# Performance work log

Measured on AMD Instinct MI355X. Metric: run time of the kernel, lower is better.

The kernel has to match this reference:

```python
import jax, jax.numpy as jnp
import numpy as np

N = 100000      # nodes
E = 3_200_000   # edges
F_IN = 256      # input feature dim
R = 16          # rank_bound (GCN output dim)
D = 128         # embedding_dim (trans output)
B = 16384       # batch of node indices
EPS = 1e-5


def setup_inputs() -> dict:
    key = jax.random.key(0)
    ks = jax.random.split(key, 9)
    x = jax.random.normal(ks[0], (N, F_IN), jnp.float32)
    edge_index = jax.random.randint(ks[1], (2, E), 0, N, dtype=jnp.int64)
    trans = jax.random.normal(ks[2], (R, D), jnp.float32) * 0.1
    batch = jax.random.randint(ks[3], (B,), 0, N, dtype=jnp.int64)
    W = jax.random.normal(ks[4], (R, F_IN), jnp.float32) / np.sqrt(F_IN).astype(np.float32)
    b = jnp.zeros((R,), jnp.float32)
    ln_w = jnp.ones((R,), jnp.float32)
    ln_b = jnp.zeros((R,), jnp.float32)
    prelu_a = jnp.full((1,), 0.25, jnp.float32)  # PReLU single shared slope
    return dict(x=x, edge_index=edge_index, trans=trans, batch=batch,
                W=W, b=b, ln_w=ln_w, ln_b=ln_b, prelu_a=prelu_a)


def gcn_conv(x, edge_index, W, b):
    # PyG GCNConv: lin first, then symmetric-normalized aggregation with self-loops.
    h = x @ W.T  # [N, R]
    loop = jnp.arange(N, dtype=edge_index.dtype)
    src = jnp.concatenate([edge_index[0], loop])  # messages flow src -> dst
    dst = jnp.concatenate([edge_index[1], loop])
    deg = jax.ops.segment_sum(jnp.ones_like(dst, h.dtype), dst, num_segments=N)
    dinv = jnp.where(deg > 0, jax.lax.rsqrt(deg), 0.0)
    norm = dinv[src] * dinv[dst]                   # [E+N]
    msg = h[src] * norm[:, None]                   # gather [E+N, R]
    out = jax.ops.segment_sum(msg, dst, num_segments=N)  # scatter-add
    return out + b


def reference(x, edge_index, trans, batch, W, b, ln_w, ln_b, prelu_a):
    h = gcn_conv(x, edge_index, W, b)              # [N, R]
    # PyG LayerNorm (graph mode): normalize over all nodes and channels.
    h = h - h.mean()
    var = (h * h).mean()
    h = h * jax.lax.rsqrt(var + EPS) * ln_w + ln_b
    # PReLU
    h = jnp.where(h >= 0, h, prelu_a * h)
    emb = h @ trans                                # [N, D]
    return emb[batch]                              # index_select(0, batch)
```

## Files before the change

### kernel.cpp

```cpp
#include <hip/hip_runtime.h>

#define EPS 1e-5f
#define BSHIFT 8
#define BSIZE  256
#define NBMAX  512
#define PCHUNK 8192
#define LCAP   12288

typedef short bf16x8 __attribute__((ext_vector_type(8)));
typedef float f32x4  __attribute__((ext_vector_type(4)));

__device__ __forceinline__ unsigned short f2bf(float f) {
    unsigned u = __float_as_uint(f);
    u += 0x7FFFu + ((u >> 16) & 1u);
    return (unsigned short)(u >> 16);
}
__device__ __forceinline__ float bf2f(unsigned short s) {
    return __uint_as_float(((unsigned)s) << 16);
}
__device__ __forceinline__ void acc8(float* acc, uint4 v) {
    acc[0] += bf2f((unsigned short)(v.x & 0xFFFFu)); acc[1] += bf2f((unsigned short)(v.x >> 16));
    acc[2] += bf2f((unsigned short)(v.y & 0xFFFFu)); acc[3] += bf2f((unsigned short)(v.y >> 16));
    acc[4] += bf2f((unsigned short)(v.z & 0xFFFFu)); acc[5] += bf2f((unsigned short)(v.z >> 16));
    acc[6] += bf2f((unsigned short)(v.w & 0xFFFFu)); acc[7] += bf2f((unsigned short)(v.w >> 16));
}
__device__ __forceinline__ void cvt_hilo(const float* f, bf16x8& hi, bf16x8& lo) {
#pragma unroll
    for (int j = 0; j < 8; j++) {
        unsigned short h = f2bf(f[j]);
        hi[j] = (short)h;
        lo[j] = (short)f2bf(f[j] - bf2f(h));
    }
}
__device__ __forceinline__ void gload_lds16(const float* g, float* l) {
    __builtin_amdgcn_global_load_lds((const __attribute__((address_space(1))) void*)g,
                                     (__attribute__((address_space(3))) void*)l, 16, 0, 0);
}

__global__ __launch_bounds__(512) void k_zero(unsigned* ghist, int NB) {
    int t = threadIdx.x;
    if (t < NB) ghist[t] = 0u;
}

__global__ __launch_bounds__(512) void k_bhist(const int* __restrict__ ei,
                                               unsigned* __restrict__ ghist,
                                               unsigned* __restrict__ blkhist,
                                               int E, int NB) {
    __shared__ unsigned sh[NBMAX];
    int t = threadIdx.x;
    for (int i = t; i < NB; i += 512) sh[i] = 0u;
    __syncthreads();
    const int4* dst4 = (const int4*)(ei + E);
    int E4 = E >> 2;
    int base4 = blockIdx.x * (PCHUNK / 4);
#pragma unroll
    for (int i = 0; i < PCHUNK / 4 / 512; i++) {
        int idx = base4 + i * 512 + t;
        if (idx < E4) {
            int4 d = dst4[idx];
            atomicAdd(&sh[d.x >> BSHIFT], 1u);
            atomicAdd(&sh[d.y >> BSHIFT], 1u);
            atomicAdd(&sh[d.z >> BSHIFT], 1u);
            atomicAdd(&sh[d.w >> BSHIFT], 1u);
        }
    }
    __syncthreads();
    unsigned* bh = blkhist + (size_t)blockIdx.x * NBMAX;
    for (int i = t; i < NB; i += 512) {
        unsigned c = sh[i];
        bh[i] = c;
        if (c) atomicAdd(&ghist[i], c);
    }
}

__global__ __launch_bounds__(512) void k_bscan(const unsigned* __restrict__ ghist,
                                               unsigned* __restrict__ base,
                                               unsigned* __restrict__ cursor,
                                               unsigned* __restrict__ nstart,
                                               int NB, int N, int E) {
    __shared__ unsigned sh[512];
    int t = threadIdx.x;
    unsigned v = (t < NB) ? ghist[t] : 0u;
    sh[t] = v;
    __syncthreads();
    for (int off = 1; off < 512; off <<= 1) {
        unsigned a = (t >= off) ? sh[t - off] : 0u;
        __syncthreads();
        sh[t] += a;
        __syncthreads();
    }
    if (t < NB) { unsigned ex = sh[t] - v; base[t] = ex; cursor[t] = ex; }
    if (t == 0) { base[NB] = (unsigned)E; nstart[N] = (unsigned)E; }
}

__global__ __launch_bounds__(512) void k_bpart(const int* __restrict__ ei,
                                               const unsigned* __restrict__ blkhist,
                                               unsigned* __restrict__ cursor,
                                               unsigned* __restrict__ sorted, int E, int NB) {
    __shared__ unsigned cnt[NBMAX];
    __shared__ unsigned lbase[NBMAX];
    __shared__ unsigned loff[NBMAX + 1];
    __shared__ unsigned sh[512];
    __shared__ unsigned stage[PCHUNK];
    __shared__ unsigned short bkt[PCHUNK];
    int t = threadIdx.x;
    const unsigned* bh = blkhist + (size_t)blockIdx.x * NBMAX;
    for (int i = t; i < NB; i += 512) cnt[i] = bh[i];
    __syncthreads();
    const int4* src4 = (const int4*)ei;
    const int4* dst4 = (const int4*)(ei + E);
    int E4 = E >> 2;
    int base4 = blockIdx.x * (PCHUNK / 4);
    unsigned v = (t < NB) ? cnt[t] : 0u;
    sh[t] = v;
    if (t < NB) lbase[t] = v ? atomicAdd(&cursor[t], v) : 0u;
    __syncthreads();
    for (int off = 1; off < 512; off <<= 1) {
        unsigned a = (t >= off) ? sh[t - off] : 0u;
        __syncthreads();
        sh[t] += a;
        __syncthreads();
    }
    if (t < NB) { loff[t] = sh[t] - v; cnt[t] = 0u; }
    if (t == NB - 1) loff[NB] = sh[t];
    __syncthreads();
    for (int b = t; b < NB; b += 512) {
        unsigned s = loff[b], e2 = loff[b + 1];
        for (unsigned j = s; j < e2; j++) bkt[j] = (unsigned short)b;
    }
#pragma unroll
    for (int i = 0; i < PCHUNK / 4 / 512; i++) {
        int idx = base4 + i * 512 + t;
        if (idx < E4) {
            int4 s = src4[idx];
            int4 d = dst4[idx];
            int b; unsigned r;
            b = d.x >> BSHIFT; r = atomicAdd(&cnt[b], 1u);
            stage[loff[b] + r] = (unsigned)s.x | ((unsigned)(d.x & (BSIZE - 1)) << 17);
            b = d.y >> BSHIFT; r = atomicAdd(&cnt[b], 1u);
            stage[loff[b] + r] = (unsigned)s.y | ((unsigned)(d.y & (BSIZE - 1)) << 17);
            b = d.z >> BSHIFT; r = atomicAdd(&cnt[b], 1u);
            stage[loff[b] + r] = (unsigned)s.z | ((unsigned)(d.z & (BSIZE - 1)) << 17);
            b = d.w >> BSHIFT; r = atomicAdd(&cnt[b], 1u);
            stage[loff[b] + r] = (unsigned)s.w | ((unsigned)(d.w & (BSIZE - 1)) << 17);
        }
    }
    __syncthreads();
    unsigned total = loff[NB];
    for (unsigned i = t; i < total; i += 512) {
        unsigned b = bkt[i];
        sorted[lbase[b] + (i - loff[b])] = stage[i];
    }
}

__global__ __launch_bounds__(256) void k_bdeg2(const unsigned* __restrict__ base,
                                               const unsigned* __restrict__ sorted,
                                               unsigned* __restrict__ nstart,
                                               float* __restrict__ dinv, int N) {
    __shared__ unsigned deg[BSIZE];
    int b = blockIdx.x, t = threadIdx.x;
    deg[t] = 0u;
    __syncthreads();
    unsigned s0 = base[b], s1 = base[b + 1];
    for (unsigned j = s0 + t; j < s1; j += 256)
        atomicAdd(&deg[sorted[j] >> 17], 1u);
    __syncthreads();
    unsigned d0 = deg[t];
    int lane = t & 63, wid = t >> 6;
    unsigned inc = d0;
    for (int off = 1; off < 64; off <<= 1) {
        unsigned u = __shfl_up(inc, off, 64);
        if (lane >= off) inc += u;
    }
    __shared__ unsigned wsum[4];
    if (lane == 63) wsum[wid] = inc;
    __syncthreads();
    unsigned wbase = 0;
    for (int w = 0; w < wid; w++) wbase += wsum[w];
    unsigned excl = wbase + inc - d0;
    int node = (b << BSHIFT) + t;
    if (node < N) {
        nstart[node] = s0 + excl;
        dinv[node] = rsqrtf((float)(d0 + 1u));
    }
}

__global__ __launch_bounds__(256) void k_gemm(const float* __restrict__ x,
                                              const float* __restrict__ W,
                                              const float* __restrict__ dinv,
                                              unsigned short* __restrict__ hs,
                                              int N, int NCH) {
    __shared__ float xs[64][260];
    int t = threadIdx.x;
    int w = t >> 6, lane = t & 63;
    int lr = lane & 15;
    int lk = lane >> 4;
    bf16x8 bh[8], bl[8];
#pragma unroll
    for (int kt = 0; kt < 8; kt++) {
        float wf[8];
        const float* wp = W + lr * 256 + kt * 32 + lk * 8;
        *(float4*)&wf[0] = *(const float4*)wp;
        *(float4*)&wf[4] = *(const float4*)(wp + 4);
        cvt_hilo(wf, bh[kt], bl[kt]);
    }
    for (int ch = blockIdx.x; ch < NCH; ch += gridDim.x) {
        int cb = ch << 6;
#pragma unroll
        for (int j = 0; j < 16; j++) {
            int row = w * 16 + j;
            int node = cb + row;
            if (node < N)
                gload_lds16(x + (size_t)node * 256 + lane * 4, &xs[row][0]);
        }
        __syncthreads();
        f32x4 acc = {0.f, 0.f, 0.f, 0.f};
#pragma unroll
        for (int kt = 0; kt < 8; kt++) {
            float af[8];
            const float* ap = &xs[w * 16 + lr][kt * 32 + lk * 8];
            *(float4*)&af[0] = *(const float4*)ap;
            *(float4*)&af[4] = *(const float4*)(ap + 4);
            bf16x8 ah, al;
            cvt_hilo(af, ah, al);
            acc = __builtin_amdgcn_mfma_f32_16x16x32_bf16(ah, bh[kt], acc, 0, 0, 0);
            acc = __builtin_amdgcn_mfma_f32_16x16x32_bf16(al, bh[kt], acc, 0, 0, 0);
            acc = __builtin_amdgcn_mfma_f32_16x16x32_bf16(ah, bl[kt], acc, 0, 0, 0);
        }
#pragma unroll
        for (int i = 0; i < 4; i++) {
            int node = cb + w * 16 + lk * 4 + i;
            if (node < N) {
                float dv = dinv[node];
                hs[(size_t)node * 16 + lr] = f2bf(acc[i] * dv);
            }
        }
        __syncthreads();
    }
}

__global__ __launch_bounds__(256) void k_aggf(const unsigned* __restrict__ base,
                                              const unsigned* __restrict__ nstart,
                                              const unsigned* __restrict__ sorted,
                                              const unsigned short* __restrict__ hs,
                                              const float* __restrict__ dinv,
                                              const float* __restrict__ bias,
                                              float* __restrict__ agg,
                                              float2* __restrict__ part,
                                              unsigned* __restrict__ scratch, int N) {
    __shared__ unsigned buf[LCAP];
    __shared__ unsigned cur0[BSIZE + 1];
    __shared__ unsigned curv[BSIZE];
    __shared__ float ss[4], qq[4];
    int b = blockIdx.x, t = threadIdx.x;
    unsigned s0 = base[b], s1 = base[b + 1];
    unsigned len = s1 - s0;
    int node = (b << BSHIFT) + t;
    unsigned ns = (node < N) ? nstart[node] : s1;
    cur0[t] = ns - s0;
    curv[t] = ns - s0;
    if (t == 0) cur0[BSIZE] = len;
    __syncthreads();
    bool fit = (len <= (unsigned)LCAP);
    if (fit) {
        for (unsigned j = t; j < len; j += 256) {
            unsigned u = sorted[s0 + j];
            unsigned pos = atomicAdd(&curv[u >> 17], 1u);
            buf[pos] = u & 0x1FFFFu;
        }
    } else {
        for (unsigned j = t; j < len; j += 256) {
            unsigned u = sorted[s0 + j];
            unsigned pos = atomicAdd(&curv[u >> 17], 1u);
            scratch[s0 + pos] = u & 0x1FFFFu;
        }
    }
    __syncthreads();
    int g = t >> 4, r = t & 15;
    int sub = r >> 1;
    int half = r & 1;
    float sacc = 0.f, qacc = 0.f;
#pragma unroll 1
    for (int p = 0; p < 16; p++) {
        int dloc = p * 16 + g;
        int d = (b << BSHIFT) + dloc;
        float acc[8];
#pragma unroll
        for (int c = 0; c < 8; c++) acc[c] = 0.f;
        if (d < N) {
            unsigned l0 = cur0[dloc], l1 = cur0[dloc + 1];
            for (unsigned j = l0; j < l1; j += 16) {
                unsigned row0 = j + sub, row1 = j + 8 + sub;
                bool p0 = row0 < l1, p1 = row1 < l1;
                unsigned i0 = 0, i1 = 0;
                if (fit) {
                    if (p0) i0 = buf[row0];
                    if (p1) i1 = buf[row1];
                } else {
                    if (p0) i0 = scratch[s0 + row0];
                    if (p1) i1 = scratch[s0 + row1];
                }
                uint4 v0, v1;
                if (p0) v0 = ((const uint4*)(hs + (size_t)i0 * 16))[half];
                if (p1) v1 = ((const uint4*)(hs + (size_t)i1 * 16))[half];
                if (p0) acc8(acc, v0);
                if (p1) acc8(acc, v1);
            }
        }
#pragma unroll
        for (int off = 2; off <= 8; off <<= 1) {
#pragma unroll
            for (int c = 0; c < 8; c++) acc[c] += __shfl_down(acc[c], off, 64);
        }
        if (d < N && r < 2) {
            float dd = dinv[d];
            uint4 hv = ((const uint4*)(hs + (size_t)d * 16))[half];
            float self[8];
            self[0] = bf2f((unsigned short)(hv.x & 0xFFFFu)); self[1] = bf2f((unsigned short)(hv.x >> 16));
            self[2] = bf2f((unsigned short)(hv.y & 0xFFFFu)); self[3] = bf2f((unsigned short)(hv.y >> 16));
            self[4] = bf2f((unsigned short)(hv.z & 0xFFFFu)); self[5] = bf2f((unsigned short)(hv.z >> 16));
            self[6] = bf2f((unsigned short)(hv.w & 0xFFFFu)); self[7] = bf2f((unsigned short)(hv.w >> 16));
            float o[8];
#pragma unroll
            for (int c = 0; c < 8; c++) o[c] = (acc[c] + self[c]) * dd;
            float* an = agg + (size_t)d * 16 + half * 8;
            *(float4*)(an)     = make_float4(o[0], o[1], o[2], o[3]);
            *(float4*)(an + 4) = make_float4(o[4], o[5], o[6], o[7]);
            const float* bp = bias + half * 8;
            float4 b0 = *(const float4*)bp, b1 = *(const float4*)(bp + 4);
            float a0 = o[0] + b0.x, a1 = o[1] + b0.y, a2 = o[2] + b0.z, a3 = o[3] + b0.w;
            float a4 = o[4] + b1.x, a5 = o[5] + b1.y, a6 = o[6] + b1.z, a7 = o[7] + b1.w;
            sacc += (a0 + a1) + (a2 + a3) + (a4 + a5) + (a6 + a7);
            qacc += a0 * a0 + a1 * a1 + a2 * a2 + a3 * a3 + a4 * a4 + a5 * a5 + a6 * a6 + a7 * a7;
        }
    }
    for (int off = 32; off > 0; off >>= 1) {
        sacc += __shfl_down(sacc, off, 64);
        qacc += __shfl_down(qacc, off, 64);
    }
    int lane = t & 63, wid = t >> 6;
    if (lane == 0) { ss[wid] = sacc; qq[wid] = qacc; }
    __syncthreads();
    if (t == 0)
        part[b] = make_float2(ss[0] + ss[1] + ss[2] + ss[3],
                              qq[0] + qq[1] + qq[2] + qq[3]);
}

__global__ __launch_bounds__(256) void k_statsred(const float2* __restrict__ part,
                                                  float* __restrict__ scal, int M) {
    int t = threadIdx.x;
    float s = 0.f, q = 0.f;
    for (int i = t; i < M; i += 256) {
        float2 v = part[i];
        s += v.x; q += v.y;
    }
    for (int off = 32; off > 0; off >>= 1) {
        s += __shfl_down(s, off, 64);
        q += __shfl_down(q, off, 64);
    }
    __shared__ float ss[4], qq[4];
    int lane = t & 63, wid = t >> 6;
    if (lane == 0) { ss[wid] = s; qq[wid] = q; }
    __syncthreads();
    if (t == 0) {
        scal[0] = ss[0] + ss[1] + ss[2] + ss[3];
        scal[1] = qq[0] + qq[1] + qq[2] + qq[3];
    }
}

__global__ __launch_bounds__(256) void k_final(const float* __restrict__ agg,
                                               const int* __restrict__ batch,
                                               const float* __restrict__ trans,
                                               const float* __restrict__ bias,
                                               const float* __restrict__ ln_w,
                                               const float* __restrict__ ln_b,
                                               const float* __restrict__ prelu_a,
                                               const float* __restrict__ scal,
                                               float* __restrict__ out, int B, float invCnt) {
    __shared__ float tl[16 * 128];
    __shared__ float hh[8 * 16];
    const int tid = threadIdx.x;
    for (int i = tid; i < 2048; i += 256) tl[i] = trans[i];
    float mean = scal[0] * invCnt;
    float var  = scal[1] * invCnt - mean * mean;
    float inv  = rsqrtf(var + EPS);
    int row0 = blockIdx.x * 8;
    if (tid < 128) {
        int lr = tid >> 4, r = tid & 15;
        int row = row0 + lr;
        if (row < B) {
            int node = batch[row];
            float v = agg[(size_t)node * 16 + r] + bias[r];
            v = (v - mean) * inv * ln_w[r] + ln_b[r];
            float a = prelu_a[0];
            v = v >= 0.f ? v : a * v;
            hh[lr * 16 + r] = v;
        }
    }
    __syncthreads();
    int d = tid & 127, hlf = tid >> 7;
    float tv[16];
#pragma unroll
    for (int r = 0; r < 16; r++) tv[r] = tl[r * 128 + d];
#pragma unroll
    for (int rr = 0; rr < 4; rr++) {
        int lr = rr * 2 + hlf;
        int row = row0 + lr;
        if (row < B) {
            const float* hrow = hh + lr * 16;
            float acc = 0.f;
#pragma unroll
            for (int r = 0; r < 16; r++) acc += hrow[r] * tv[r];
            out[(size_t)row * 128 + d] = acc;
        }
    }
}

extern "C" void kernel_launch(void* const* d_in, const int* in_sizes, int n_in,
                              void* d_out, int out_size, void* d_ws, size_t ws_size,
                              hipStream_t stream) {
    const float* x       = (const float*)d_in[0];
    const int*   ei      = (const int*)d_in[1];
    const float* trans   = (const float*)d_in[2];
    const int*   batch   = (const int*)d_in[3];
    const float* W       = (const float*)d_in[4];
    const float* bias    = (const float*)d_in[5];
    const float* ln_w    = (const float*)d_in[6];
    const float* ln_b    = (const float*)d_in[7];
    const float* prelu_a = (const float*)d_in[8];
    float* out = (float*)d_out;

    const int N = in_sizes[0] / 256;
    const int E = in_sizes[1] / 2;
    const int B = in_sizes[3];
    const int NB = (N + BSIZE - 1) >> BSHIFT;
    const int pbp = (E + PCHUNK - 1) / PCHUNK;
    const int NCH = (N + 63) / 64;

    char* p = (char*)d_ws;
    unsigned short* hs = (unsigned short*)p;  p += (size_t)N * 16 * 2;
    float*    agg     = (float*)p;     p += (size_t)N * 16 * 4;
    unsigned* sorted  = (unsigned*)p;  p += (size_t)E * 4;
    unsigned* scratch = (unsigned*)p;  p += (size_t)E * 4;
    unsigned* blkhist = (unsigned*)p;  p += (size_t)pbp * NBMAX * 4;
    float*    dinv    = (float*)p;     p += (size_t)N * 4;
    unsigned* nstart  = (unsigned*)p;  p += (size_t)(N + 1) * 4;
    unsigned* ghist   = (unsigned*)p;  p += NBMAX * 4;
    unsigned* base    = (unsigned*)p;  p += (NBMAX + 1) * 4;
    unsigned* cursor  = (unsigned*)p;  p += NBMAX * 4;
    float*    scal    = (float*)p;     p += 2 * 4;
    p = (char*)(((size_t)p + 7) & ~(size_t)7);
    float2*   part    = (float2*)p;    p += (size_t)NB * 8;

    hipLaunchKernelGGL(k_zero,     dim3(1),               dim3(512), 0, stream, ghist, NB);
    hipLaunchKernelGGL(k_bhist,    dim3(pbp),             dim3(512), 0, stream, ei, ghist, blkhist, E, NB);
    hipLaunchKernelGGL(k_bscan,    dim3(1),               dim3(512), 0, stream, ghist, base, cursor, nstart, NB, N, E);
    hipLaunchKernelGGL(k_bpart,    dim3(pbp),             dim3(512), 0, stream, ei, blkhist, cursor, sorted, E, NB);
    hipLaunchKernelGGL(k_bdeg2,    dim3(NB),              dim3(256), 0, stream, base, sorted, nstart, dinv, N);
    hipLaunchKernelGGL(k_gemm,     dim3(512),             dim3(256), 0, stream, x, W, dinv, hs, N, NCH);
    hipLaunchKernelGGL(k_aggf,     dim3(NB),              dim3(256), 0, stream, base, nstart, sorted, hs, dinv, bias, agg, part, scratch, N);
    hipLaunchKernelGGL(k_statsred, dim3(1),               dim3(256), 0, stream, part, scal, NB);
    hipLaunchKernelGGL(k_final,    dim3((B + 7) / 8),     dim3(256), 0, stream, agg, batch, trans, bias,
                       ln_w, ln_b, prelu_a, scal, out, B, 1.0f / (float)(N * 16));
}
```

Before: 292.6 us.

## Widen degree and aggregation blocks to 512 threads; per-wave GEMM with direct loads

The degree and aggregation kernels now run with 512 threads per 256-node bucket, so twice as many threads share the edge-bucketing and gather work and each thread covers half as many destination groups. The GEMM drops its LDS staging and block-wide barriers: each wave independently owns 16-row tiles and reads x straight from global memory into registers, with launch bounds set for higher occupancy. The aim is more latency hiding and no barrier stalls, at the cost of larger register footprints and possibly less coalesced x reads in the GEMM.

```diff
diff --git a/kernel.cpp b/kernel.cpp
--- a/kernel.cpp
+++ b/kernel.cpp
@@ -31,10 +31,6 @@
         hi[j] = (short)h;
         lo[j] = (short)f2bf(f[j] - bf2f(h));
     }
-}
-__device__ __forceinline__ void gload_lds16(const float* g, float* l) {
-    __builtin_amdgcn_global_load_lds((const __attribute__((address_space(1))) void*)g,
-                                     (__attribute__((address_space(3))) void*)l, 16, 0, 0);
 }
 
 __global__ __launch_bounds__(512) void k_zero(unsigned* ghist, int NB) {
@@ -153,44 +149,48 @@
     }
 }
 
-__global__ __launch_bounds__(256) void k_bdeg2(const unsigned* __restrict__ base,
+__global__ __launch_bounds__(512) void k_bdeg2(const unsigned* __restrict__ base,
                                                const unsigned* __restrict__ sorted,
                                                unsigned* __restrict__ nstart,
                                                float* __restrict__ dinv, int N) {
     __shared__ unsigned deg[BSIZE];
+    __shared__ unsigned wsum[4];
     int b = blockIdx.x, t = threadIdx.x;
-    deg[t] = 0u;
+    if (t < BSIZE) deg[t] = 0u;
     __syncthreads();
     unsigned s0 = base[b], s1 = base[b + 1];
-    for (unsigned j = s0 + t; j < s1; j += 256)
+    for (unsigned j = s0 + t; j < s1; j += 512)
         atomicAdd(&deg[sorted[j] >> 17], 1u);
     __syncthreads();
-    unsigned d0 = deg[t];
+    unsigned d0 = 0, inc = 0;
     int lane = t & 63, wid = t >> 6;
-    unsigned inc = d0;
-    for (int off = 1; off < 64; off <<= 1) {
-        unsigned u = __shfl_up(inc, off, 64);
-        if (lane >= off) inc += u;
-    }
-    __shared__ unsigned wsum[4];
-    if (lane == 63) wsum[wid] = inc;
-    __syncthreads();
-    unsigned wbase = 0;
-    for (int w = 0; w < wid; w++) wbase += wsum[w];
-    unsigned excl = wbase + inc - d0;
-    int node = (b << BSHIFT) + t;
-    if (node < N) {
-        nstart[node] = s0 + excl;
-        dinv[node] = rsqrtf((float)(d0 + 1u));
-    }
-}
-
-__global__ __launch_bounds__(256) void k_gemm(const float* __restrict__ x,
-                                              const float* __restrict__ W,
-                                              const float* __restrict__ dinv,
-                                              unsigned short* __restrict__ hs,
-                                              int N, int NCH) {
-    __shared__ float xs[64][260];
+    if (t < BSIZE) {
+        d0 = deg[t];
+        inc = d0;
+        for (int off = 1; off < 64; off <<= 1) {
+            unsigned u = __shfl_up(inc, off, 64);
+            if (lane >= off) inc += u;
+        }
+        if (lane == 63) wsum[wid] = inc;
+    }
+    __syncthreads();
+    if (t < BSIZE) {
+        unsigned wbase = 0;
+        for (int w = 0; w < wid; w++) wbase += wsum[w];
+        unsigned excl = wbase + inc - d0;
+        int node = (b << BSHIFT) + t;
+        if (node < N) {
+            nstart[node] = s0 + excl;
+            dinv[node] = rsqrtf((float)(d0 + 1u));
+        }
+    }
+}
+
+__global__ __launch_bounds__(256, 4) void k_gemm(const float* __restrict__ x,
+                                                 const float* __restrict__ W,
+                                                 const float* __restrict__ dinv,
+                                                 unsigned short* __restrict__ hs,
+                                                 int N, int NT) {
     int t = threadIdx.x;
     int w = t >> 6, lane = t & 63;
     int lr = lane & 15;
@@ -204,23 +204,24 @@
         *(float4*)&wf[4] = *(const float4*)(wp + 4);
         cvt_hilo(wf, bh[kt], bl[kt]);
     }
-    for (int ch = blockIdx.x; ch < NCH; ch += gridDim.x) {
-        int cb = ch << 6;
-#pragma unroll
-        for (int j = 0; j < 16; j++) {
-            int row = w * 16 + j;
-            int node = cb + row;
-            if (node < N)
-                gload_lds16(x + (size_t)node * 256 + lane * 4, &xs[row][0]);
-        }
-        __syncthreads();
+    int nw = gridDim.x * 4;
+    int wid = blockIdx.x * 4 + w;
+    for (int tile = wid; tile < NT; tile += nw) {
+        int nb = tile << 4;
+        int node = nb + lr;
+        const float* xp = x + (size_t)node * 256;
         f32x4 acc = {0.f, 0.f, 0.f, 0.f};
 #pragma unroll
         for (int kt = 0; kt < 8; kt++) {
             float af[8];
-            const float* ap = &xs[w * 16 + lr][kt * 32 + lk * 8];
-            *(float4*)&af[0] = *(const float4*)ap;
-            *(float4*)&af[4] = *(const float4*)(ap + 4);
+            if (node < N) {
+                const float* ap = xp + kt * 32 + lk * 8;
+                *(float4*)&af[0] = *(const float4*)ap;
+                *(float4*)&af[4] = *(const float4*)(ap + 4);
+            } else {
+#pragma unroll
+                for (int j = 0; j < 8; j++) af[j] = 0.f;
+            }
             bf16x8 ah, al;
             cvt_hilo(af, ah, al);
             acc = __builtin_amdgcn_mfma_f32_16x16x32_bf16(ah, bh[kt], acc, 0, 0, 0);
@@ -229,17 +230,16 @@
         }
 #pragma unroll
         for (int i = 0; i < 4; i++) {
-            int node = cb + w * 16 + lk * 4 + i;
-            if (node < N) {
-                float dv = dinv[node];
-                hs[(size_t)node * 16 + lr] = f2bf(acc[i] * dv);
+            int n2 = nb + lk * 4 + i;
+            if (n2 < N) {
+                float dv = dinv[n2];
+                hs[(size_t)n2 * 16 + lr] = f2bf(acc[i] * dv);
             }
         }
-        __syncthreads();
-    }
-}
-
-__global__ __launch_bounds__(256) void k_aggf(const unsigned* __restrict__ base,
+    }
+}
+
+__global__ __launch_bounds__(512) void k_aggf(const unsigned* __restrict__ base,
                                               const unsigned* __restrict__ nstart,
                                               const unsigned* __restrict__ sorted,
                                               const unsigned short* __restrict__ hs,
@@ -251,25 +251,27 @@
     __shared__ unsigned buf[LCAP];
     __shared__ unsigned cur0[BSIZE + 1];
     __shared__ unsigned curv[BSIZE];
-    __shared__ float ss[4], qq[4];
+    __shared__ float ss[8], qq[8];
     int b = blockIdx.x, t = threadIdx.x;
     unsigned s0 = base[b], s1 = base[b + 1];
     unsigned len = s1 - s0;
-    int node = (b << BSHIFT) + t;
-    unsigned ns = (node < N) ? nstart[node] : s1;
-    cur0[t] = ns - s0;
-    curv[t] = ns - s0;
+    if (t < BSIZE) {
+        int node = (b << BSHIFT) + t;
+        unsigned ns = (node < N) ? nstart[node] : s1;
+        cur0[t] = ns - s0;
+        curv[t] = ns - s0;
+    }
     if (t == 0) cur0[BSIZE] = len;
     __syncthreads();
     bool fit = (len <= (unsigned)LCAP);
     if (fit) {
-        for (unsigned j = t; j < len; j += 256) {
+        for (unsigned j = t; j < len; j += 512) {
             unsigned u = sorted[s0 + j];
             unsigned pos = atomicAdd(&curv[u >> 17], 1u);
             buf[pos] = u & 0x1FFFFu;
         }
     } else {
-        for (unsigned j = t; j < len; j += 256) {
+        for (unsigned j = t; j < len; j += 512) {
             unsigned u = sorted[s0 + j];
             unsigned pos = atomicAdd(&curv[u >> 17], 1u);
             scratch[s0 + pos] = u & 0x1FFFFu;
@@ -281,8 +283,8 @@
     int half = r & 1;
     float sacc = 0.f, qacc = 0.f;
 #pragma unroll 1
-    for (int p = 0; p < 16; p++) {
-        int dloc = p * 16 + g;
+    for (int p = 0; p < 8; p++) {
+        int dloc = p * 32 + g;
         int d = (b << BSHIFT) + dloc;
         float acc[8];
 #pragma unroll
@@ -341,9 +343,12 @@
     int lane = t & 63, wid = t >> 6;
     if (lane == 0) { ss[wid] = sacc; qq[wid] = qacc; }
     __syncthreads();
-    if (t == 0)
-        part[b] = make_float2(ss[0] + ss[1] + ss[2] + ss[3],
-                              qq[0] + qq[1] + qq[2] + qq[3]);
+    if (t == 0) {
+        float s = 0.f, q = 0.f;
+#pragma unroll
+        for (int i = 0; i < 8; i++) { s += ss[i]; q += qq[i]; }
+        part[b] = make_float2(s, q);
+    }
 }
 
 __global__ __launch_bounds__(256) void k_statsred(const float2* __restrict__ part,
@@ -435,7 +440,7 @@
     const int B = in_sizes[3];
     const int NB = (N + BSIZE - 1) >> BSHIFT;
     const int pbp = (E + PCHUNK - 1) / PCHUNK;
-    const int NCH = (N + 63) / 64;
+    const int NT = (N + 15) / 16;
 
     char* p = (char*)d_ws;
     unsigned short* hs = (unsigned short*)p;  p += (size_t)N * 16 * 2;
@@ -456,9 +461,9 @@
     hipLaunchKernelGGL(k_bhist,    dim3(pbp),             dim3(512), 0, stream, ei, ghist, blkhist, E, NB);
     hipLaunchKernelGGL(k_bscan,    dim3(1),               dim3(512), 0, stream, ghist, base, cursor, nstart, NB, N, E);
     hipLaunchKernelGGL(k_bpart,    dim3(pbp),             dim3(512), 0, stream, ei, blkhist, cursor, sorted, E, NB);
-    hipLaunchKernelGGL(k_bdeg2,    dim3(NB),              dim3(256), 0, stream, base, sorted, nstart, dinv, N);
-    hipLaunchKernelGGL(k_gemm,     dim3(512),             dim3(256), 0, stream, x, W, dinv, hs, N, NCH);
-    hipLaunchKernelGGL(k_aggf,     dim3(NB),              dim3(256), 0, stream, base, nstart, sorted, hs, dinv, bias, agg, part, scratch, N);
+    hipLaunchKernelGGL(k_bdeg2,    dim3(NB),              dim3(512), 0, stream, base, sorted, nstart, dinv, N);
+    hipLaunchKernelGGL(k_gemm,     dim3(512),             dim3(256), 0, stream, x, W, dinv, hs, N, NT);
+    hipLaunchKernelGGL(k_aggf,     dim3(NB),              dim3(512), 0, stream, base, nstart, sorted, hs, dinv, bias, agg, part, scratch, N);
     hipLaunchKernelGGL(k_statsred, dim3(1),               dim3(256), 0, stream, part, scal, NB);
     hipLaunchKernelGGL(k_final,    dim3((B + 7) / 8),     dim3(256), 0, stream, agg, batch, trans, bias,
                        ln_w, ln_b, prelu_a, scal, out, B, 1.0f / (float)(N * 16));
```

Result: faster. 279.9 us (-4.3%).
